# Performance work log

Hardware: AMD Instinct MI355X
Metric: run time of the kernel (lower is better)

Reference implementation:

```python
import jax, jax.numpy as jnp
import numpy as np

B, L, D_MODEL = 8, 2048, 768
D_INNER, D_STATE, DT_RANK, K = 1536, 16, 48, 4


def setup_inputs() -> dict:
    key = jax.random.key(0)
    ks = jax.random.split(key, 9)
    s = 0.02
    return {
        "hidden_states": jax.random.normal(ks[0], (B, L, D_MODEL), jnp.float32),
        "W_in": jax.random.normal(ks[1], (D_MODEL, 2 * D_INNER), jnp.float32) * s,
        "conv_w": jax.random.normal(ks[2], (D_INNER, 1, K), jnp.float32) * s,
        "conv_b": jax.random.normal(ks[3], (D_INNER,), jnp.float32) * s,
        "W_x": jax.random.normal(ks[4], (DT_RANK + 2 * D_STATE, D_INNER), jnp.float32) * s,
        "W_dt": jax.random.normal(ks[5], (D_INNER, DT_RANK), jnp.float32) * s,
        "b_dt": jax.random.normal(ks[6], (D_INNER,), jnp.float32) * s,
        "A_log": jax.random.normal(ks[7], (D_INNER, D_STATE), jnp.float32),
        "D_param": jax.random.normal(ks[8], (D_INNER,), jnp.float32),
    }


def _mamba(hidden_states, W_in, conv_w, conv_b, W_x, W_dt, b_dt, A_log, D_param):
    # in_proj then chunk into ssm branch (x) and gating residual (res)
    xz = hidden_states @ W_in                      # (B, L, 2*d_inner)
    x, res = jnp.split(xz, 2, axis=-1)             # each (B, L, d_inner)

    # causal depthwise conv over time, then SiLU
    xc = x.transpose(0, 2, 1)                      # (B, C, L)
    xc = jax.lax.conv_general_dilated(
        xc, conv_w, window_strides=(1,), padding=[(K - 1, 0)],
        feature_group_count=D_INNER, dimension_numbers=("NCH", "OIH", "NCH"))
    x = jax.nn.silu(xc + conv_b[None, :, None]).transpose(0, 2, 1)  # (B, L, d_inner)

    # input-dependent SSM parameters
    x_dbl = x @ W_x.T                              # (B, L, dt_rank + 2*d_state)
    dt = jax.nn.softplus(x_dbl[..., :DT_RANK] @ W_dt.T + b_dt)      # (B, L, d_inner)
    Bm = x_dbl[..., DT_RANK:DT_RANK + D_STATE]     # (B, L, d_state)
    Cm = x_dbl[..., DT_RANK + D_STATE:]            # (B, L, d_state)
    A = -jnp.exp(A_log)                            # (d_inner, d_state)

    def step(h, inp):
        x_t, dt_t, B_t, C_t = inp                  # (B,d_inner),(B,d_inner),(B,d_state),(B,d_state)
        dA = jnp.exp(dt_t[..., None] * A)          # (B, d_inner, d_state)
        dBx = (dt_t * x_t)[..., None] * B_t[:, None, :]
        h = dA * h + dBx
        y = jnp.einsum("bds,bs->bd", h, C_t)
        return h, y

    xs = (x.transpose(1, 0, 2), dt.transpose(1, 0, 2),
          Bm.transpose(1, 0, 2), Cm.transpose(1, 0, 2))
    h0 = jnp.zeros((x.shape[0], D_INNER, D_STATE), x.dtype)
    _, ys = jax.lax.scan(step, h0, xs)             # ys: (L, B, d_inner)
    y = ys.transpose(1, 0, 2) + x * D_param        # skip term
    return y * jax.nn.silu(res)                    # gated output (B, L, d_inner)


def reference(hidden_states, W_in, conv_w, conv_b, W_x, W_dt, b_dt, A_log, D_param):
    return _mamba(hidden_states, W_in, conv_w, conv_b, W_x, W_dt, b_dt, A_log, D_param)
```

## Files before the change

kernel.cpp:

```cpp
#include <hip/hip_runtime.h>
#include <hip/hip_bf16.h>
#include <stdint.h>

#define B_SZ 8
#define L_SZ 2048
#define DM 768
#define DI 1536
#define DS 16
#define DR 48
#define M_SZ (B_SZ * L_SZ)
#define N1 (2 * DI)

#define NC 32
#define TC (L_SZ / NC)
#define CH (B_SZ * DI)
#define KS 6
#define NT2 (DM / 32)
#define L2E 1.44269504088896f

typedef short short8 __attribute__((ext_vector_type(8)));
typedef float f32x4 __attribute__((ext_vector_type(4)));

__device__ __forceinline__ ushort f2b(float f) {
  __hip_bfloat16 h = __float2bfloat16(f);
  return *reinterpret_cast<ushort*>(&h);
}
__device__ __forceinline__ float b2f(ushort u) {
  __hip_bfloat16 h;
  *reinterpret_cast<ushort*>(&h) = u;
  return __bfloat162float(h);
}
__device__ __forceinline__ ushort f2h(float f) {
  _Float16 h = (_Float16)f;
  return *reinterpret_cast<ushort*>(&h);
}
__device__ __forceinline__ float h2f(ushort u) {
  _Float16 h;
  *reinterpret_cast<ushort*>(&h) = u;
  return (float)h;
}

__device__ __forceinline__ void gl16(const ushort* g, ushort* l) {
  __builtin_amdgcn_global_load_lds(
      (const __attribute__((address_space(1))) void*)g,
      (__attribute__((address_space(3))) void*)l, 16, 0, 0);
}

#define EXP4(dst, src)                                      \
  {                                                         \
    float _e0, _e1, _e2, _e3;                               \
    asm("v_exp_f32 %0, %1" : "=v"(_e0) : "v"((src)[0]));    \
    asm("v_exp_f32 %0, %1" : "=v"(_e1) : "v"((src)[1]));    \
    asm("v_exp_f32 %0, %1" : "=v"(_e2) : "v"((src)[2]));    \
    asm("v_exp_f32 %0, %1" : "=v"(_e3) : "v"((src)[3]));    \
    (dst) = f32x4{_e0, _e1, _e2, _e3};                      \
  }


__global__ __launch_bounds__(256) void prep_all(const float4* __restrict__ hs4,
                                                const float* __restrict__ w_in,
                                                const float* __restrict__ wx_f,
                                                const float* __restrict__ wdt_f,
                                                ushort4* __restrict__ A1,
                                                ushort* __restrict__ wt,
                                                ushort* __restrict__ wx_b,
                                                ushort* __restrict__ wdt_p) {
  const int n4 = M_SZ * DM / 4;
  const int nT = 3072 * 96;
  const int nwx = 80 * DI;
  const int nwdt = DI * 64;
  int idx = blockIdx.x * 256 + threadIdx.x;
  if (idx < n4) {
    float4 v = hs4[idx];
    ushort4 o;
    o.x = f2b(v.x); o.y = f2b(v.y); o.z = f2b(v.z); o.w = f2b(v.w);
    A1[idx] = o;
  } else if (idx < n4 + nT) {
    int j = idx - n4;
    int n = j % 3072;
    int kb = (j / 3072) * 8;
    short8 o;
#pragma unroll
    for (int q = 0; q < 8; ++q) o[q] = (short)f2b(w_in[(size_t)(kb + q) * 3072 + n]);
    *(short8*)(wt + (size_t)n * DM + kb) = o;
  } else if (idx < n4 + nT + nwx) {
    int j = idx - n4 - nT;
    wx_b[j] = f2b(wx_f[j]);
  } else if (idx < n4 + nT + nwx + nwdt) {
    int j = idx - n4 - nT - nwx;
    int col = j >> 6, k = j & 63;
    wdt_p[j] = (k < DR) ? f2b(wdt_f[col * DR + k]) : (ushort)0;
  }
}


__global__ __launch_bounds__(512, 1) void gemm_xz(const ushort* __restrict__ A,
                                                  const ushort* __restrict__ Bt,
                                                  ushort* __restrict__ xout,
                                                  ushort* __restrict__ gateout) {
  __shared__ ushort lds[49152];

  const int t = threadIdx.x;
  const int lane = t & 63;
  const int wid = t >> 6;
  const int wm = wid >> 2, wn = wid & 3;
  const int r = lane & 15, hi = lane >> 4;

  const int g = blockIdx.x;
  const int swz = (g & 7) * (768 / 8) + (g >> 3);
  const int bx = swz & 63;
  const int by = swz >> 6;
  const int bm = bx * 256;
  const int bn = by * 256;

  const ushort* gsrc[4];
  int ldso[4];
#pragma unroll
  for (int i = 0; i < 4; ++i) {
    int c = wid * 4 + i;
    if (c < 16)
      gsrc[i] = A + (size_t)(bm + c * 16 + r) * DM + hi * 8;
    else
      gsrc[i] = Bt + (size_t)(bn + (c - 16) * 16 + r) * DM + hi * 8;
    ldso[i] = c * 512;
  }

  f32x4 acc[8][4];
#pragma unroll
  for (int m = 0; m < 8; ++m)
#pragma unroll
    for (int n = 0; n < 4; ++n) acc[m][n] = f32x4{0.f, 0.f, 0.f, 0.f};

  ushort* b0 = lds;
  ushort* b1 = lds + 16384;
  ushort* b2 = lds + 32768;

#pragma unroll
  for (int i = 0; i < 4; ++i) gl16(gsrc[i], b0 + ldso[i]);
#pragma unroll
  for (int i = 0; i < 4; ++i) gl16(gsrc[i] + 32, b1 + ldso[i]);
  asm volatile("s_waitcnt vmcnt(4)" ::: "memory");
  __builtin_amdgcn_s_barrier();

  for (int kt = 0; kt < NT2; ++kt) {
    const bool stage = (kt + 2 < NT2);
    const int koff = (kt + 2) * 32;

    short8 bfr[4];
#pragma unroll
    for (int n = 0; n < 4; ++n)
      bfr[n] = *(const short8*)&b0[(16 + wn * 4 + n) * 512 + lane * 8];

#pragma unroll
    for (int q = 0; q < 2; ++q) {
      short8 afr[4];
#pragma unroll
      for (int m = 0; m < 4; ++m)
        afr[m] = *(const short8*)&b0[(wm * 8 + q * 4 + m) * 512 + lane * 8];

      if (stage) {
        gl16(gsrc[2 * q] + koff, b2 + ldso[2 * q]);
        gl16(gsrc[2 * q + 1] + koff, b2 + ldso[2 * q + 1]);
      }

      asm volatile("s_barrier" ::: "memory");

      __builtin_amdgcn_s_setprio(1);
#pragma unroll
      for (int m = 0; m < 4; ++m)
#pragma unroll
        for (int n = 0; n < 4; ++n)
          acc[q * 4 + m][n] =
              __builtin_amdgcn_mfma_f32_16x16x32_bf16(afr[m], bfr[n], acc[q * 4 + m][n], 0, 0, 0);
      __builtin_amdgcn_s_setprio(0);

      if (q == 1) {
        if (stage)
          asm volatile("s_waitcnt vmcnt(4)" ::: "memory");
        else
          asm volatile("s_waitcnt vmcnt(0)" ::: "memory");
      }
      asm volatile("s_barrier" ::: "memory");
    }

    ushort* tmp = b0; b0 = b1; b1 = b2; b2 = tmp;
  }

  const bool isx = (bn < DI);
  ushort* outp = isx ? xout : gateout;
  const int cbase = bn - (isx ? 0 : DI) + wn * 64;
#pragma unroll
  for (int mf = 0; mf < 8; ++mf)
#pragma unroll
    for (int nf = 0; nf < 4; ++nf) {
      int col = cbase + nf * 16 + r;
#pragma unroll
      for (int j = 0; j < 4; ++j) {
        int row = bm + wm * 128 + mf * 16 + hi * 4 + j;
        float v = acc[mf][nf][j];
        if (!isx) v = v / (1.f + __expf(-v));
        outp[(size_t)row * DI + col] = f2b(v);
      }
    }
}


__global__ __launch_bounds__(256) void conv_silu(const ushort* __restrict__ xp,
                                                 const float* __restrict__ cw,
                                                 const float* __restrict__ cb,
                                                 ushort* __restrict__ xc) {
  int tid = blockIdx.x * 256 + threadIdx.x;
  const int nd = DI / 8;
  int db = tid % nd;
  int row = tid / nd;
  int d0 = db * 8;
  int l = row & (L_SZ - 1);
  const ushort* base = xp + (size_t)row * DI + d0;
  short8 z8 = {0, 0, 0, 0, 0, 0, 0, 0};
  short8 x0 = *(const short8*)base;
  short8 xm1 = (l >= 1) ? *(const short8*)(base - DI) : z8;
  short8 xm2 = (l >= 2) ? *(const short8*)(base - 2 * DI) : z8;
  short8 xm3 = (l >= 3) ? *(const short8*)(base - 3 * DI) : z8;
  short8 o;
#pragma unroll
  for (int j = 0; j < 8; ++j) {
    float4 w = *(const float4*)(cw + (size_t)(d0 + j) * 4);
    float a = cb[d0 + j] + w.x * b2f((ushort)xm3[j]) + w.y * b2f((ushort)xm2[j]) +
              w.z * b2f((ushort)xm1[j]) + w.w * b2f((ushort)x0[j]);
    float s = a / (1.f + __expf(-a));
    o[j] = (short)f2b(s);
  }
  *(short8*)(xc + (size_t)row * DI + d0) = o;
}


__global__ __launch_bounds__(256) void xdbl_gemm(const ushort* __restrict__ xc,
                                                 const ushort* __restrict__ wx,
                                                 float* __restrict__ xdp) {
  int wave = blockIdx.x * 4 + (threadIdx.x >> 6);
  int ks = blockIdx.y;
  int lane = threadIdx.x & 63;
  int r = lane & 15, hi = lane >> 4;
  int row0 = wave * 16;
  f32x4 acc[5];
#pragma unroll
  for (int n = 0; n < 5; ++n) acc[n] = f32x4{0.f, 0.f, 0.f, 0.f};
  const int kbeg = ks * (DI / KS), kend = kbeg + DI / KS;
  for (int k0 = kbeg; k0 < kend; k0 += 32) {
    short8 a = *(const short8*)(xc + (size_t)(row0 + r) * DI + k0 + hi * 8);
#pragma unroll
    for (int n = 0; n < 5; ++n) {
      short8 b = *(const short8*)(wx + (size_t)(n * 16 + r) * DI + k0 + hi * 8);
      acc[n] = __builtin_amdgcn_mfma_f32_16x16x32_bf16(a, b, acc[n], 0, 0, 0);
    }
  }
  float* op = xdp + (size_t)ks * M_SZ * 80;
#pragma unroll
  for (int n = 0; n < 5; ++n)
#pragma unroll
    for (int j = 0; j < 4; ++j)
      op[(size_t)(row0 + hi * 4 + j) * 80 + n * 16 + r] = acc[n][j];
}

__global__ __launch_bounds__(256) void reduce_xd(const float4* __restrict__ xdp,
                                                 float4* __restrict__ xd) {
  int i = blockIdx.x * 256 + threadIdx.x;
  if (i >= M_SZ * 20) return;
  float4 s = xdp[i];
#pragma unroll
  for (int k = 1; k < KS; ++k) {
    float4 v = xdp[(size_t)k * M_SZ * 20 + i];
    s.x += v.x; s.y += v.y; s.z += v.z; s.w += v.w;
  }
  xd[i] = s;
}


__device__ __forceinline__ short8 pack8f(const float* p) {
  short8 v;
#pragma unroll
  for (int i = 0; i < 8; ++i) v[i] = (short)f2b(p[i]);
  return v;
}

__global__ __launch_bounds__(256) void dt_gemm(const float* __restrict__ xd,
                                               const ushort* __restrict__ wdtp,
                                               const float* __restrict__ bdt,
                                               ushort* __restrict__ dt) {
  int wave = blockIdx.x * 4 + (threadIdx.x >> 6);
  int lane = threadIdx.x & 63;
  int r = lane & 15, hi = lane >> 4;
  int row0 = wave * 16;
  int c0 = blockIdx.y * 64;

  float atmp[8];
  const float* ap = xd + (size_t)(row0 + r) * 80 + hi * 8;
  float4 q0 = *(const float4*)ap, q1 = *(const float4*)(ap + 4);
  atmp[0] = q0.x; atmp[1] = q0.y; atmp[2] = q0.z; atmp[3] = q0.w;
  atmp[4] = q1.x; atmp[5] = q1.y; atmp[6] = q1.z; atmp[7] = q1.w;
  short8 a0 = pack8f(atmp);
  short8 a1 = {0, 0, 0, 0, 0, 0, 0, 0};
  if (hi < 2) {
    const float* ap1 = xd + (size_t)(row0 + r) * 80 + 32 + hi * 8;
    float4 p0 = *(const float4*)ap1, p1 = *(const float4*)(ap1 + 4);
    atmp[0] = p0.x; atmp[1] = p0.y; atmp[2] = p0.z; atmp[3] = p0.w;
    atmp[4] = p1.x; atmp[5] = p1.y; atmp[6] = p1.z; atmp[7] = p1.w;
    a1 = pack8f(atmp);
  }

  f32x4 acc[4];
#pragma unroll
  for (int n = 0; n < 4; ++n) acc[n] = f32x4{0.f, 0.f, 0.f, 0.f};
#pragma unroll
  for (int n = 0; n < 4; ++n) {
    const ushort* wp = wdtp + (size_t)(c0 + n * 16 + r) * 64;
    short8 b0 = *(const short8*)(wp + hi * 8);
    short8 b1 = *(const short8*)(wp + 32 + hi * 8);
    acc[n] = __builtin_amdgcn_mfma_f32_16x16x32_bf16(a0, b0, acc[n], 0, 0, 0);
    acc[n] = __builtin_amdgcn_mfma_f32_16x16x32_bf16(a1, b1, acc[n], 0, 0, 0);
  }
#pragma unroll
  for (int n = 0; n < 4; ++n)
#pragma unroll
    for (int j = 0; j < 4; ++j) {
      int col = c0 + n * 16 + r;
      float z = acc[n][j] + bdt[col];
      float sp = (z > 20.f) ? z : __logf(1.f + __expf(z));
      dt[(size_t)(row0 + hi * 4 + j) * DI + col] = f2h(sp);
    }
}


__global__ __launch_bounds__(256) void scan_pass1(const ushort* __restrict__ dt,
                                                  const ushort* __restrict__ xc,
                                                  const float* __restrict__ xd,
                                                  const float* __restrict__ A_log,
                                                  float* __restrict__ hend,
                                                  float* __restrict__ sumdt) {
  const int d = blockIdx.x * 256 + threadIdx.x;
  const int c = blockIdx.y, b = blockIdx.z;
  const int t0 = c * TC;

  __shared__ float Bs[TC * 16];
  for (int i = threadIdx.x; i < TC * 16; i += 256) {
    int tt = i >> 4, s = i & 15;
    Bs[i] = xd[((size_t)(b * L_SZ + t0 + tt)) * 80 + DR + s];
  }

  f32x4 a4[4];
  const float4* al4 = (const float4*)(A_log + (size_t)d * DS);
#pragma unroll
  for (int q = 0; q < 4; ++q) {
    float4 v = al4[q];
    a4[q] = f32x4{-__expf(v.x) * L2E, -__expf(v.y) * L2E,
                  -__expf(v.z) * L2E, -__expf(v.w) * L2E};
  }

  __syncthreads();

  f32x4 h4[4];
#pragma unroll
  for (int q = 0; q < 4; ++q) h4[q] = f32x4{0.f, 0.f, 0.f, 0.f};
  float sd = 0.f;

  const ushort* dtp = dt + ((size_t)b * L_SZ + t0) * DI + d;
  const ushort* xp = xc + ((size_t)b * L_SZ + t0) * DI + d;

  ushort dtu_n = *dtp;
  ushort xu_n = *xp;
  const f32x4* bp4 = (const f32x4*)Bs;
  for (int tt = 0; tt < TC; ++tt) {
    dtp += DI; xp += DI;
    ushort dtu = dtu_n;
    ushort xu = xu_n;
    dtu_n = *dtp;
    xu_n = *xp;
    float dtv = h2f(dtu);
    float xv = b2f(xu);
    sd += dtv;
    float dx = dtv * xv;
    f32x4 dts = f32x4{dtv, dtv, dtv, dtv};
    f32x4 dxs = f32x4{dx, dx, dx, dx};
#pragma unroll
    for (int q = 0; q < 4; ++q) {
      f32x4 arg = dts * a4[q];
      f32x4 dA;
      EXP4(dA, arg);
      h4[q] = dA * h4[q] + dxs * bp4[q];
    }
    bp4 += 4;
  }

  const size_t ch = (size_t)b * DI + d;
  sumdt[ch * NC + c] = sd;
  f32x4* hp = (f32x4*)&hend[((size_t)c * CH + ch) * 16];
#pragma unroll
  for (int q = 0; q < 4; ++q) hp[q] = h4[q];
}

__global__ __launch_bounds__(256) void scan_pass2(const float* __restrict__ A_log,
                                                  const float* __restrict__ sumdt,
                                                  const float* __restrict__ hend,
                                                  float* __restrict__ hstart) {
  int idx = blockIdx.x * 256 + threadIdx.x;
  int ch = idx >> 4, s = idx & 15;
  int d = ch % DI;
  float A = -__expf(A_log[d * DS + s]);
  float h = 0.f;
  for (int c = 0; c < NC; ++c) {
    hstart[((size_t)c * CH + ch) * 16 + s] = h;
    float sd = sumdt[(size_t)ch * NC + c];
    h = __expf(A * sd) * h + hend[((size_t)c * CH + ch) * 16 + s];
  }
}

__global__ __launch_bounds__(256) void scan_pass3(const ushort* __restrict__ dt,
                                                  const ushort* __restrict__ xc,
                                                  const float* __restrict__ xd,
                                                  const ushort* __restrict__ gateb,
                                                  const float* __restrict__ A_log,
                                                  const float* __restrict__ Dp,
                                                  const float* __restrict__ hstart,
                                                  float* __restrict__ out) {
  const int d = blockIdx.x * 256 + threadIdx.x;
  const int c = blockIdx.y, b = blockIdx.z;
  const int t0 = c * TC;

  __shared__ float Bs[TC * 16];
  __shared__ float Cs[TC * 16];
  for (int i = threadIdx.x; i < TC * 16; i += 256) {
    int tt = i >> 4, s = i & 15;
    size_t row = ((size_t)(b * L_SZ + t0 + tt)) * 80;
    Bs[i] = xd[row + DR + s];
    Cs[i] = xd[row + DR + DS + s];
  }

  f32x4 a4[4];
  const float4* al4 = (const float4*)(A_log + (size_t)d * DS);
#pragma unroll
  for (int q = 0; q < 4; ++q) {
    float4 v = al4[q];
    a4[q] = f32x4{-__expf(v.x) * L2E, -__expf(v.y) * L2E,
                  -__expf(v.z) * L2E, -__expf(v.w) * L2E};
  }
  const float Dpv = Dp[d];

  const size_t ch = (size_t)b * DI + d;
  f32x4 h4[4];
  const f32x4* hp = (const f32x4*)&hstart[((size_t)c * CH + ch) * 16];
#pragma unroll
  for (int q = 0; q < 4; ++q) h4[q] = hp[q];

  __syncthreads();

  const ushort* dtp = dt + ((size_t)b * L_SZ + t0) * DI + d;
  const ushort* xp = xc + ((size_t)b * L_SZ + t0) * DI + d;
  const ushort* gp = gateb + ((size_t)b * L_SZ + t0) * DI + d;
  float* op = out + ((size_t)b * L_SZ + t0) * DI + d;

  ushort dtu_n = *dtp;
  ushort xu_n = *xp;
  ushort gu_n = *gp;
  const f32x4* bp4 = (const f32x4*)Bs;
  const f32x4* cp4 = (const f32x4*)Cs;
  for (int tt = 0; tt < TC; ++tt) {
    dtp += DI; xp += DI; gp += DI;
    ushort dtu = dtu_n;
    ushort xu = xu_n;
    ushort gu = gu_n;
    dtu_n = *dtp;
    xu_n = *xp;
    gu_n = *gp;
    float dtv = h2f(dtu);
    float xv = b2f(xu);
    float gv = b2f(gu);
    float dx = dtv * xv;
    f32x4 dts = f32x4{dtv, dtv, dtv, dtv};
    f32x4 dxs = f32x4{dx, dx, dx, dx};
    f32x4 y4 = f32x4{0.f, 0.f, 0.f, 0.f};
#pragma unroll
    for (int q = 0; q < 4; ++q) {
      f32x4 arg = dts * a4[q];
      f32x4 dA;
      EXP4(dA, arg);
      h4[q] = dA * h4[q] + dxs * bp4[q];
      y4 = y4 + h4[q] * cp4[q];
    }
    bp4 += 4; cp4 += 4;
    float y = (y4[0] + y4[1]) + (y4[2] + y4[3]);
    op[0] = (y + xv * Dpv) * gv;
    op += DI;
  }
}


extern "C" void kernel_launch(void* const* d_in, const int* in_sizes, int n_in,
                              void* d_out, int out_size, void* d_ws, size_t ws_size,
                              hipStream_t stream) {
  const float* hs     = (const float*)d_in[0];
  const float* W_in   = (const float*)d_in[1];
  const float* conv_w = (const float*)d_in[2];
  const float* conv_b = (const float*)d_in[3];
  const float* W_x    = (const float*)d_in[4];
  const float* W_dt   = (const float*)d_in[5];
  const float* b_dt   = (const float*)d_in[6];
  const float* A_log  = (const float*)d_in[7];
  const float* D_par  = (const float*)d_in[8];
  float* out = (float*)d_out;
  char* ws = (char*)d_ws;

  size_t o = 0;
  ushort* A1   = (ushort*)(ws + o); o += (size_t)M_SZ * DM * 2;
  ushort* Wt1  = (ushort*)(ws + o); o += (size_t)N1 * DM * 2;
  ushort* xpre = (ushort*)(ws + o); o += (size_t)M_SZ * DI * 2;
  ushort* gate = (ushort*)(ws + o); o += (size_t)M_SZ * DI * 2;
  ushort* xcv  = (ushort*)(ws + o); o += (size_t)M_SZ * DI * 2;
  float*  xdbl = (float*)(ws + o);  o += (size_t)M_SZ * 80 * 4;
  ushort* dtb  = (ushort*)(ws + o); o += (size_t)M_SZ * DI * 2;
  float*  xdp  = (float*)(ws + o);  o += (size_t)KS * M_SZ * 80 * 4;
  ushort* Wxb  = (ushort*)(ws + o); o += (size_t)80 * DI * 2;
  ushort* Wdtp = (ushort*)(ws + o); o += (size_t)DI * 64 * 2;
  if (ws_size < o) return;

  float* hend   = (float*)(ws + 0);
  float* hstart = (float*)(ws + (size_t)NC * CH * 16 * 4);
  float* sumdt  = (float*)(ws + (size_t)2 * NC * CH * 16 * 4);

  const int nprep = M_SZ * DM / 4 + 3072 * 96 + 80 * DI + DI * 64;
  prep_all<<<dim3((nprep + 255) / 256), dim3(256), 0, stream>>>(
      (const float4*)hs, W_in, W_x, W_dt, (ushort4*)A1, Wt1, Wxb, Wdtp);

  gemm_xz<<<dim3((M_SZ / 256) * (N1 / 256)), dim3(512), 0, stream>>>(A1, Wt1, xpre, gate);

  conv_silu<<<dim3(M_SZ * DI / 8 / 256), dim3(256), 0, stream>>>(xpre, conv_w, conv_b, xcv);

  xdbl_gemm<<<dim3(M_SZ / 64, KS), dim3(256), 0, stream>>>(xcv, Wxb, xdp);
  reduce_xd<<<dim3((M_SZ * 20 + 255) / 256), dim3(256), 0, stream>>>((const float4*)xdp, (float4*)xdbl);

  dt_gemm<<<dim3(M_SZ / 64, 24), dim3(256), 0, stream>>>(xdbl, Wdtp, b_dt, dtb);

  scan_pass1<<<dim3(DI / 256, NC, B_SZ), dim3(256), 0, stream>>>(dtb, xcv, xdbl, A_log, hend, sumdt);
  scan_pass2<<<dim3(CH * 16 / 256), dim3(256), 0, stream>>>(A_log, sumdt, hend, hstart);
  scan_pass3<<<dim3(DI / 256, NC, B_SZ), dim3(256), 0, stream>>>(dtb, xcv, xdbl, gate,
                                                                 A_log, D_par, hstart, out);
}
```

Measured before the change: 421.0 us.

## Shrink gemm_xz N-tile to 128 and use packed-f32 math in scan kernels

The in_proj GEMM moves from a 256x256 to a 256x128 tile with less LDS and fewer accumulators, doubling the grid. Launch bounds now allow up to four blocks per CU, aiming at higher occupancy. The two scan kernels switch from 4-wide float vectors to 2-wide vectors driven by inline v_pk_mul_f32 and v_pk_fma_f32 asm, with the time loop unrolled by two, to cut VALU issue slots in the recurrence. The smaller tile lowers data reuse per block and so raises memory traffic.

```diff
diff --git a/kernel.cpp b/kernel.cpp
--- a/kernel.cpp
+++ b/kernel.cpp
@@ -20,6 +20,7 @@
 
 typedef short short8 __attribute__((ext_vector_type(8)));
 typedef float f32x4 __attribute__((ext_vector_type(4)));
+typedef float f32x2 __attribute__((ext_vector_type(2)));
 
 __device__ __forceinline__ ushort f2b(float f) {
   __hip_bfloat16 h = __float2bfloat16(f);
@@ -45,16 +46,6 @@
       (const __attribute__((address_space(1))) void*)g,
       (__attribute__((address_space(3))) void*)l, 16, 0, 0);
 }
-
-#define EXP4(dst, src)                                      \
-  {                                                         \
-    float _e0, _e1, _e2, _e3;                               \
-    asm("v_exp_f32 %0, %1" : "=v"(_e0) : "v"((src)[0]));    \
-    asm("v_exp_f32 %0, %1" : "=v"(_e1) : "v"((src)[1]));    \
-    asm("v_exp_f32 %0, %1" : "=v"(_e2) : "v"((src)[2]));    \
-    asm("v_exp_f32 %0, %1" : "=v"(_e3) : "v"((src)[3]));    \
-    (dst) = f32x4{_e0, _e1, _e2, _e3};                      \
-  }
 
 
 __global__ __launch_bounds__(256) void prep_all(const float4* __restrict__ hs4,
@@ -94,11 +85,11 @@
 }
 
 
-__global__ __launch_bounds__(512, 1) void gemm_xz(const ushort* __restrict__ A,
+__global__ __launch_bounds__(512, 4) void gemm_xz(const ushort* __restrict__ A,
                                                   const ushort* __restrict__ Bt,
                                                   ushort* __restrict__ xout,
                                                   ushort* __restrict__ gateout) {
-  __shared__ ushort lds[49152];
+  __shared__ ushort lds[36864];
 
   const int t = threadIdx.x;
   const int lane = t & 63;
@@ -107,17 +98,17 @@
   const int r = lane & 15, hi = lane >> 4;
 
   const int g = blockIdx.x;
-  const int swz = (g & 7) * (768 / 8) + (g >> 3);
+  const int swz = (g & 7) * 192 + (g >> 3);
   const int bx = swz & 63;
   const int by = swz >> 6;
   const int bm = bx * 256;
-  const int bn = by * 256;
-
-  const ushort* gsrc[4];
-  int ldso[4];
-#pragma unroll
-  for (int i = 0; i < 4; ++i) {
-    int c = wid * 4 + i;
+  const int bn = by * 128;
+
+  const ushort* gsrc[3];
+  int ldso[3];
+#pragma unroll
+  for (int i = 0; i < 3; ++i) {
+    int c = wid * 3 + i;
     if (c < 16)
       gsrc[i] = A + (size_t)(bm + c * 16 + r) * DM + hi * 8;
     else
@@ -125,31 +116,31 @@
     ldso[i] = c * 512;
   }
 
-  f32x4 acc[8][4];
+  f32x4 acc[8][2];
 #pragma unroll
   for (int m = 0; m < 8; ++m)
 #pragma unroll
-    for (int n = 0; n < 4; ++n) acc[m][n] = f32x4{0.f, 0.f, 0.f, 0.f};
+    for (int n = 0; n < 2; ++n) acc[m][n] = f32x4{0.f, 0.f, 0.f, 0.f};
 
   ushort* b0 = lds;
-  ushort* b1 = lds + 16384;
-  ushort* b2 = lds + 32768;
-
-#pragma unroll
-  for (int i = 0; i < 4; ++i) gl16(gsrc[i], b0 + ldso[i]);
-#pragma unroll
-  for (int i = 0; i < 4; ++i) gl16(gsrc[i] + 32, b1 + ldso[i]);
-  asm volatile("s_waitcnt vmcnt(4)" ::: "memory");
+  ushort* b1 = lds + 12288;
+  ushort* b2 = lds + 24576;
+
+#pragma unroll
+  for (int i = 0; i < 3; ++i) gl16(gsrc[i], b0 + ldso[i]);
+#pragma unroll
+  for (int i = 0; i < 3; ++i) gl16(gsrc[i] + 32, b1 + ldso[i]);
+  asm volatile("s_waitcnt vmcnt(3)" ::: "memory");
   __builtin_amdgcn_s_barrier();
 
   for (int kt = 0; kt < NT2; ++kt) {
     const bool stage = (kt + 2 < NT2);
     const int koff = (kt + 2) * 32;
 
-    short8 bfr[4];
-#pragma unroll
-    for (int n = 0; n < 4; ++n)
-      bfr[n] = *(const short8*)&b0[(16 + wn * 4 + n) * 512 + lane * 8];
+    short8 bfr[2];
+#pragma unroll
+    for (int n = 0; n < 2; ++n)
+      bfr[n] = *(const short8*)&b0[(16 + wn * 2 + n) * 512 + lane * 8];
 
 #pragma unroll
     for (int q = 0; q < 2; ++q) {
@@ -159,8 +150,12 @@
         afr[m] = *(const short8*)&b0[(wm * 8 + q * 4 + m) * 512 + lane * 8];
 
       if (stage) {
-        gl16(gsrc[2 * q] + koff, b2 + ldso[2 * q]);
-        gl16(gsrc[2 * q + 1] + koff, b2 + ldso[2 * q + 1]);
+        if (q == 0) {
+          gl16(gsrc[0] + koff, b2 + ldso[0]);
+          gl16(gsrc[1] + koff, b2 + ldso[1]);
+        } else {
+          gl16(gsrc[2] + koff, b2 + ldso[2]);
+        }
       }
 
       asm volatile("s_barrier" ::: "memory");
@@ -169,14 +164,14 @@
 #pragma unroll
       for (int m = 0; m < 4; ++m)
 #pragma unroll
-        for (int n = 0; n < 4; ++n)
+        for (int n = 0; n < 2; ++n)
           acc[q * 4 + m][n] =
               __builtin_amdgcn_mfma_f32_16x16x32_bf16(afr[m], bfr[n], acc[q * 4 + m][n], 0, 0, 0);
       __builtin_amdgcn_s_setprio(0);
 
       if (q == 1) {
         if (stage)
-          asm volatile("s_waitcnt vmcnt(4)" ::: "memory");
+          asm volatile("s_waitcnt vmcnt(3)" ::: "memory");
         else
           asm volatile("s_waitcnt vmcnt(0)" ::: "memory");
       }
@@ -188,11 +183,11 @@
 
   const bool isx = (bn < DI);
   ushort* outp = isx ? xout : gateout;
-  const int cbase = bn - (isx ? 0 : DI) + wn * 64;
+  const int cbase = bn - (isx ? 0 : DI) + wn * 32;
 #pragma unroll
   for (int mf = 0; mf < 8; ++mf)
 #pragma unroll
-    for (int nf = 0; nf < 4; ++nf) {
+    for (int nf = 0; nf < 2; ++nf) {
       int col = cbase + nf * 16 + r;
 #pragma unroll
       for (int j = 0; j < 4; ++j) {
@@ -347,20 +342,20 @@
     Bs[i] = xd[((size_t)(b * L_SZ + t0 + tt)) * 80 + DR + s];
   }
 
-  f32x4 a4[4];
+  f32x2 a2[8];
   const float4* al4 = (const float4*)(A_log + (size_t)d * DS);
 #pragma unroll
   for (int q = 0; q < 4; ++q) {
     float4 v = al4[q];
-    a4[q] = f32x4{-__expf(v.x) * L2E, -__expf(v.y) * L2E,
-                  -__expf(v.z) * L2E, -__expf(v.w) * L2E};
+    a2[2 * q] = f32x2{-__expf(v.x) * L2E, -__expf(v.y) * L2E};
+    a2[2 * q + 1] = f32x2{-__expf(v.z) * L2E, -__expf(v.w) * L2E};
   }
 
   __syncthreads();
 
-  f32x4 h4[4];
-#pragma unroll
-  for (int q = 0; q < 4; ++q) h4[q] = f32x4{0.f, 0.f, 0.f, 0.f};
+  f32x2 h2[8];
+#pragma unroll
+  for (int q = 0; q < 8; ++q) h2[q] = f32x2{0.f, 0.f};
   float sd = 0.f;
 
   const ushort* dtp = dt + ((size_t)b * L_SZ + t0) * DI + d;
@@ -368,7 +363,8 @@
 
   ushort dtu_n = *dtp;
   ushort xu_n = *xp;
-  const f32x4* bp4 = (const f32x4*)Bs;
+  const f32x2* bp2 = (const f32x2*)Bs;
+#pragma unroll 2
   for (int tt = 0; tt < TC; ++tt) {
     dtp += DI; xp += DI;
     ushort dtu = dtu_n;
@@ -379,23 +375,28 @@
     float xv = b2f(xu);
     sd += dtv;
     float dx = dtv * xv;
-    f32x4 dts = f32x4{dtv, dtv, dtv, dtv};
-    f32x4 dxs = f32x4{dx, dx, dx, dx};
-#pragma unroll
-    for (int q = 0; q < 4; ++q) {
-      f32x4 arg = dts * a4[q];
-      f32x4 dA;
-      EXP4(dA, arg);
-      h4[q] = dA * h4[q] + dxs * bp4[q];
+    f32x2 dts = f32x2{dtv, dtv};
+    f32x2 dxs = f32x2{dx, dx};
+#pragma unroll
+    for (int q = 0; q < 8; ++q) {
+      f32x2 bv = bp2[q];
+      f32x2 arg, t2;
+      asm("v_pk_mul_f32 %0, %1, %2" : "=v"(arg) : "v"(dts), "v"(a2[q]));
+      float e0, e1;
+      asm("v_exp_f32 %0, %1" : "=v"(e0) : "v"(arg[0]));
+      asm("v_exp_f32 %0, %1" : "=v"(e1) : "v"(arg[1]));
+      asm("v_pk_mul_f32 %0, %1, %2" : "=v"(t2) : "v"(dxs), "v"(bv));
+      h2[q][0] = __builtin_fmaf(e0, h2[q][0], t2[0]);
+      h2[q][1] = __builtin_fmaf(e1, h2[q][1], t2[1]);
     }
-    bp4 += 4;
+    bp2 += 8;
   }
 
   const size_t ch = (size_t)b * DI + d;
   sumdt[ch * NC + c] = sd;
-  f32x4* hp = (f32x4*)&hend[((size_t)c * CH + ch) * 16];
-#pragma unroll
-  for (int q = 0; q < 4; ++q) hp[q] = h4[q];
+  f32x2* hp = (f32x2*)&hend[((size_t)c * CH + ch) * 16];
+#pragma unroll
+  for (int q = 0; q < 8; ++q) hp[q] = h2[q];
 }
 
 __global__ __launch_bounds__(256) void scan_pass2(const float* __restrict__ A_log,
@@ -435,21 +436,21 @@
     Cs[i] = xd[row + DR + DS + s];
   }
 
-  f32x4 a4[4];
+  f32x2 a2[8];
   const float4* al4 = (const float4*)(A_log + (size_t)d * DS);
 #pragma unroll
   for (int q = 0; q < 4; ++q) {
     float4 v = al4[q];
-    a4[q] = f32x4{-__expf(v.x) * L2E, -__expf(v.y) * L2E,
-                  -__expf(v.z) * L2E, -__expf(v.w) * L2E};
+    a2[2 * q] = f32x2{-__expf(v.x) * L2E, -__expf(v.y) * L2E};
+    a2[2 * q + 1] = f32x2{-__expf(v.z) * L2E, -__expf(v.w) * L2E};
   }
   const float Dpv = Dp[d];
 
   const size_t ch = (size_t)b * DI + d;
-  f32x4 h4[4];
-  const f32x4* hp = (const f32x4*)&hstart[((size_t)c * CH + ch) * 16];
-#pragma unroll
-  for (int q = 0; q < 4; ++q) h4[q] = hp[q];
+  f32x2 h2[8];
+  const f32x2* hp = (const f32x2*)&hstart[((size_t)c * CH + ch) * 16];
+#pragma unroll
+  for (int q = 0; q < 8; ++q) h2[q] = hp[q];
 
   __syncthreads();
 
@@ -461,8 +462,9 @@
   ushort dtu_n = *dtp;
   ushort xu_n = *xp;
   ushort gu_n = *gp;
-  const f32x4* bp4 = (const f32x4*)Bs;
-  const f32x4* cp4 = (const f32x4*)Cs;
+  const f32x2* bp2 = (const f32x2*)Bs;
+  const f32x2* cp2 = (const f32x2*)Cs;
+#pragma unroll 2
   for (int tt = 0; tt < TC; ++tt) {
     dtp += DI; xp += DI; gp += DI;
     ushort dtu = dtu_n;
@@ -475,19 +477,28 @@
     float xv = b2f(xu);
     float gv = b2f(gu);
     float dx = dtv * xv;
-    f32x4 dts = f32x4{dtv, dtv, dtv, dtv};
-    f32x4 dxs = f32x4{dx, dx, dx, dx};
-    f32x4 y4 = f32x4{0.f, 0.f, 0.f, 0.f};
-#pragma unroll
-    for (int q = 0; q < 4; ++q) {
-      f32x4 arg = dts * a4[q];
-      f32x4 dA;
-      EXP4(dA, arg);
-      h4[q] = dA * h4[q] + dxs * bp4[q];
-      y4 = y4 + h4[q] * cp4[q];
+    f32x2 dts = f32x2{dtv, dtv};
+    f32x2 dxs = f32x2{dx, dx};
+    f32x2 ya = f32x2{0.f, 0.f}, yb = f32x2{0.f, 0.f};
+#pragma unroll
+    for (int q = 0; q < 8; ++q) {
+      f32x2 bv = bp2[q];
+      f32x2 cv = cp2[q];
+      f32x2 arg, t2;
+      asm("v_pk_mul_f32 %0, %1, %2" : "=v"(arg) : "v"(dts), "v"(a2[q]));
+      float e0, e1;
+      asm("v_exp_f32 %0, %1" : "=v"(e0) : "v"(arg[0]));
+      asm("v_exp_f32 %0, %1" : "=v"(e1) : "v"(arg[1]));
+      asm("v_pk_mul_f32 %0, %1, %2" : "=v"(t2) : "v"(dxs), "v"(bv));
+      h2[q][0] = __builtin_fmaf(e0, h2[q][0], t2[0]);
+      h2[q][1] = __builtin_fmaf(e1, h2[q][1], t2[1]);
+      if (q & 1)
+        asm("v_pk_fma_f32 %0, %1, %2, %0" : "+v"(yb) : "v"(h2[q]), "v"(cv));
+      else
+        asm("v_pk_fma_f32 %0, %1, %2, %0" : "+v"(ya) : "v"(h2[q]), "v"(cv));
     }
-    bp4 += 4; cp4 += 4;
-    float y = (y4[0] + y4[1]) + (y4[2] + y4[3]);
+    bp2 += 8; cp2 += 8;
+    float y = (ya[0] + ya[1]) + (yb[0] + yb[1]);
     op[0] = (y + xv * Dpv) * gv;
     op += DI;
   }
@@ -530,7 +541,7 @@
   prep_all<<<dim3((nprep + 255) / 256), dim3(256), 0, stream>>>(
       (const float4*)hs, W_in, W_x, W_dt, (ushort4*)A1, Wt1, Wxb, Wdtp);
 
-  gemm_xz<<<dim3((M_SZ / 256) * (N1 / 256)), dim3(512), 0, stream>>>(A1, Wt1, xpre, gate);
+  gemm_xz<<<dim3((M_SZ / 256) * (N1 / 128)), dim3(512), 0, stream>>>(A1, Wt1, xpre, gate);
 
   conv_silu<<<dim3(M_SZ * DI / 8 / 256), dim3(256), 0, stream>>>(xpre, conv_w, conv_b, xcv);
 
```

Result: slower. 447.7 us (+6.3%).
